# Performance work log

Measured on AMD Instinct MI355X. Metric: run time of the kernel, lower is better.

Reference implementation:

```python
import jax, jax.numpy as jnp
import numpy as np

E = 256      # embedding_dim
H = 8        # num_heads
D = E // H   # head_dim = 32
F = 1024     # dim_feedforward
EPS = 1e-5


def layer_norm(x, gamma, beta):
    mu = jnp.mean(x, axis=-1, keepdims=True)
    var = jnp.var(x, axis=-1, keepdims=True)
    return (x - mu) * jax.lax.rsqrt(var + EPS) * gamma + beta


def setup_inputs() -> dict:
    key = jax.random.key(0)
    ks = jax.random.split(key, 12)
    s = lambda fan_in: 1.0 / np.sqrt(fan_in)
    src = jax.random.normal(ks[0], (4, 2048, E), dtype=jnp.float32)
    w_in = jax.random.uniform(ks[1], (3 * E, E), minval=-s(E), maxval=s(E), dtype=jnp.float32)
    w_out = jax.random.uniform(ks[2], (E, E), minval=-s(E), maxval=s(E), dtype=jnp.float32)
    w1 = jax.random.uniform(ks[3], (F, E), minval=-s(E), maxval=s(E), dtype=jnp.float32)
    b1 = jax.random.uniform(ks[4], (F,), minval=-s(E), maxval=s(E), dtype=jnp.float32)
    w2 = jax.random.uniform(ks[5], (E, F), minval=-s(F), maxval=s(F), dtype=jnp.float32)
    b2 = jax.random.uniform(ks[6], (E,), minval=-s(F), maxval=s(F), dtype=jnp.float32)
    g1 = jnp.ones((E,), jnp.float32)
    beta1 = jnp.zeros((E,), jnp.float32)
    g2 = jnp.ones((E,), jnp.float32)
    beta2 = jnp.zeros((E,), jnp.float32)
    return {"src": src, "w_in": w_in, "w_out": w_out, "w1": w1, "b1": b1,
            "w2": w2, "b2": b2, "g1": g1, "beta1": beta1, "g2": g2, "beta2": beta2}


def reference(src, w_in, w_out, w1, b1, w2, b2, g1, beta1, g2, beta2):
    B, S, _ = src.shape
    scale = D ** (-0.5)
    # --- pre-norm self-attention block ---
    x = layer_norm(src, g1, beta1)                 # [B,S,E]
    qkv = x @ w_in.T                               # [B,S,3E]
    q, k, v = jnp.split(qkv, 3, axis=-1)
    q = q.reshape(B, S, H, D).transpose(0, 2, 1, 3)  # [B,H,S,D]
    k = k.reshape(B, S, H, D).transpose(0, 2, 1, 3)
    v = v.reshape(B, S, H, D).transpose(0, 2, 1, 3)
    scores = jnp.einsum('bhqd,bhkd->bhqk', q, k) * scale  # [B,H,S,S]
    attn = jax.nn.softmax(scores, axis=-1)
    out = jnp.einsum('bhqk,bhkd->bhqd', attn, v)   # [B,H,S,D]
    out = out.transpose(0, 2, 1, 3).reshape(B, S, E)
    src = src + out @ w_out.T
    # --- pre-norm FFN block ---
    y = layer_norm(src, g2, beta2)
    y = jax.nn.relu(y @ w1.T + b1) @ w2.T + b2
    return src + y
```

## Files before the change

### kernel.cpp

```cpp
#include <hip/hip_runtime.h>
#include <hip/hip_bf16.h>
#include <math.h>

typedef unsigned short u16;
typedef unsigned int   u32;
using bf16x8 = __attribute__((ext_vector_type(8))) short;
using f32x4  = __attribute__((ext_vector_type(4))) float;
using f32x16 = __attribute__((ext_vector_type(16))) float;
using u32v4  = __attribute__((ext_vector_type(4))) u32;

#define TE 256
#define TH 8
#define TS 2048
#define TB 4
#define NTOK 8192
#define QSCALE 0.2550120651552454f
#define EXP2(x) __builtin_amdgcn_exp2f(x)

__device__ __forceinline__ void async16(const u16* g, u16* l) {
    __builtin_amdgcn_global_load_lds(
        (const __attribute__((address_space(1))) u32*)g,
        (__attribute__((address_space(3))) u32*)l, 16, 0, 0);
}
__device__ __forceinline__ u32 pkbf(float a, float b) {
    u32 ua = __float_as_uint(a) + 0x8000u;
    u32 ub = __float_as_uint(b) + 0x8000u;
    return __builtin_amdgcn_perm(ub, ua, 0x07060302u);
}
__device__ __forceinline__ u16 bf1(float a) {
    return (u16)((__float_as_uint(a) + 0x8000u) >> 16);
}
template<int N> __device__ __forceinline__ void waitv() {
    if constexpr (N == 0)      asm volatile("s_waitcnt vmcnt(0)" ::: "memory");
    else if constexpr (N == 2) asm volatile("s_waitcnt vmcnt(2)" ::: "memory");
    else                       asm volatile("s_waitcnt vmcnt(4)" ::: "memory");
}

__global__ __launch_bounds__(256) void ln_bf(const float* __restrict__ in,
        u16* __restrict__ out, const float* __restrict__ gamma,
        const float* __restrict__ beta) {
    int row  = blockIdx.x * 4 + (threadIdx.x >> 6);
    int lane = threadIdx.x & 63;
    float4 v = ((const float4*)(in + (size_t)row * TE))[lane];
    float s  = v.x + v.y + v.z + v.w;
    float s2 = v.x*v.x + v.y*v.y + v.z*v.z + v.w*v.w;
    #pragma unroll
    for (int off = 32; off > 0; off >>= 1) {
        s  += __shfl_down(s,  off, 64);
        s2 += __shfl_down(s2, off, 64);
    }
    s  = __shfl(s,  0, 64);
    s2 = __shfl(s2, 0, 64);
    float mu = s * (1.f / TE);
    float rs = rsqrtf(s2 * (1.f / TE) - mu * mu + 1e-5f);
    float4 g = ((const float4*)gamma)[lane];
    float4 b = ((const float4*)beta )[lane];
    u32 lo = pkbf((v.x - mu) * rs * g.x + b.x, (v.y - mu) * rs * g.y + b.y);
    u32 hi = pkbf((v.z - mu) * rs * g.z + b.z, (v.w - mu) * rs * g.w + b.w);
    ((uint2*)(out + (size_t)row * TE))[lane] = make_uint2(lo, hi);
}

__global__ __launch_bounds__(256) void convw(const float* __restrict__ s0, u16* d0,
        const float* __restrict__ s1, u16* d1, const float* __restrict__ s2, u16* d2,
        const float* __restrict__ s3, u16* d3) {
    int i = (blockIdx.x * 256 + threadIdx.x) * 4;
    const float* s; u16* d;
    if      (i < 196608) { s = s0; d = d0; }
    else if (i < 262144) { s = s1; d = d1; i -= 196608; }
    else if (i < 524288) { s = s2; d = d2; i -= 262144; }
    else                 { s = s3; d = d3; i -= 524288; }
    float4 v = *(const float4*)(s + i);
    *(uint2*)(d + i) = make_uint2(pkbf(v.x, v.y), pkbf(v.z, v.w));
}

template<int K, int BM, int EPI>
__global__ __launch_bounds__(256) void mgemm(const u16* __restrict__ A,
        const u16* __restrict__ W, const float* __restrict__ bias,
        const float* __restrict__ R, float* __restrict__ Cf,
        u16* __restrict__ Cb, int M) {
    constexpr int BN = BM;
    constexpr int NS = K / 32;
    constexpr int L  = (BM == 128) ? 4 : 2;
    __shared__ u16 Al[3][BM * 32];
    __shared__ u16 Wl[3][BN * 32];
    const int tid = threadIdx.x, w = tid >> 6, l = tid & 63;
    const int n0 = blockIdx.y * BM;
    const int m0 = blockIdx.x * BN;
    constexpr int NT = (BM == 128) ? 4 : 2;
    constexpr int NF = (BM == 128) ? 4 : 2;
    const int tw = (w & 1) * NT * 16;
    const int fw = (w >> 1) * NF * 16;
    const int fr = l & 15, fq = l >> 4;
    const int sr = l >> 2, sc = (l & 3) * 8;
    f32x4 acc[NT][NF];
    #pragma unroll
    for (int t = 0; t < NT; t++)
        #pragma unroll
        for (int f = 0; f < NF; f++)
            #pragma unroll
            for (int r = 0; r < 4; r++) acc[t][f][r] = 0.f;

    auto stage = [&](int s, int buf) {
        const int kc = s * 32;
        if constexpr (BM == 128) {
            #pragma unroll
            for (int c = 0; c < 2; c++) {
                const int rr = (w * 2 + c) * 16 + sr;
                async16(A + (size_t)(n0 + rr) * K + kc + sc, &Al[buf][(w * 2 + c) * 512]);
                async16(W + (size_t)(m0 + rr) * K + kc + sc, &Wl[buf][(w * 2 + c) * 512]);
            }
        } else {
            const int rr = w * 16 + sr;
            async16(A + (size_t)(n0 + rr) * K + kc + sc, &Al[buf][w * 512]);
            async16(W + (size_t)(m0 + rr) * K + kc + sc, &Wl[buf][w * 512]);
        }
    };

    stage(0, 0);
    stage(1, 1);
    #pragma unroll
    for (int s = 0; s < NS; ++s) {
        const int buf = s % 3;
        if (s < NS - 1) waitv<L>();
        else            waitv<0>();
        __builtin_amdgcn_s_barrier();
        __builtin_amdgcn_sched_barrier(0);
        if (s + 2 < NS) stage(s + 2, (s + 2) % 3);
        bf16x8 af[NT], wf[NF];
        #pragma unroll
        for (int t = 0; t < NT; t++)
            af[t] = *(const bf16x8*)&Al[buf][(tw + t * 16 + fr) * 32 + fq * 8];
        #pragma unroll
        for (int f = 0; f < NF; f++)
            wf[f] = *(const bf16x8*)&Wl[buf][(fw + f * 16 + fr) * 32 + fq * 8];
        #pragma unroll
        for (int t = 0; t < NT; t++)
            #pragma unroll
            for (int f = 0; f < NF; f++)
                acc[t][f] = __builtin_amdgcn_mfma_f32_16x16x32_bf16(
                    wf[f], af[t], acc[t][f], 0, 0, 0);
    }
    #pragma unroll
    for (int t = 0; t < NT; t++) {
        const int tok = n0 + tw + t * 16 + fr;
        #pragma unroll
        for (int f = 0; f < NF; f++) {
            const int fb = m0 + fw + f * 16 + fq * 4;
            f32x4 v = acc[t][f];
            if (EPI == 0) {
                if (fb < 256) {
                    *(uint2*)(Cb + (size_t)tok * 256 + fb) = make_uint2(
                        pkbf(v[0]*QSCALE, v[1]*QSCALE), pkbf(v[2]*QSCALE, v[3]*QSCALE));
                } else if (fb < 512) {
                    const int hh = (fb - 256) >> 5, dd = (fb - 256) & 31;
                    const int bh = (tok >> 11) * 8 + hh;
                    const int kv = tok & 2047, tile = kv >> 5, lq = kv & 31;
                    const int fg = dd >> 4, hg = (dd >> 3) & 1, j = dd & 7;
                    u16* kp = (u16*)bias +
                        (((((size_t)bh * 64 + tile) * 2 + fg) * 2 + hg) * 32 + lq) * 8 + j;
                    *(uint2*)kp = make_uint2(pkbf(v[0], v[1]), pkbf(v[2], v[3]));
                } else {
                    const int hh = (fb - 512) >> 5, dd = (fb - 512) & 31;
                    const int bh = (tok >> 11) * 8 + hh;
                    const int kv = tok & 2047, tile = kv >> 5, kvr = kv & 31;
                    const int fg = kvr >> 4, hg = (kvr >> 3) & 1, j = kvr & 7;
                    u16* vp = (u16*)R +
                        ((((size_t)bh * 64 + tile) * 2 + fg) * 2 + hg) * 256 +
                        (size_t)dd * 8 + j;
                    vp[0]  = bf1(v[0]);
                    vp[8]  = bf1(v[1]);
                    vp[16] = bf1(v[2]);
                    vp[24] = bf1(v[3]);
                }
            } else if (EPI == 1) {
                float4 r4 = *(const float4*)(R + (size_t)tok * M + fb);
                *(float4*)(Cf + (size_t)tok * M + fb) =
                    make_float4(v[0]+r4.x, v[1]+r4.y, v[2]+r4.z, v[3]+r4.w);
            } else if (EPI == 2) {
                float4 b4 = *(const float4*)(bias + fb);
                *(uint2*)(Cb + (size_t)tok * M + fb) = make_uint2(
                    pkbf(fmaxf(v[0]+b4.x, 0.f), fmaxf(v[1]+b4.y, 0.f)),
                    pkbf(fmaxf(v[2]+b4.z, 0.f), fmaxf(v[3]+b4.w, 0.f)));
            } else {
                float4 b4 = *(const float4*)(bias + fb);
                float4 r4 = *(const float4*)(R + (size_t)tok * M + fb);
                *(float4*)(Cf + (size_t)tok * M + fb) = make_float4(
                    v[0]+b4.x+r4.x, v[1]+b4.y+r4.y, v[2]+b4.z+r4.z, v[3]+b4.w+r4.w);
            }
        }
    }
}

__global__ __launch_bounds__(256, 4) void attn_k(const u16* __restrict__ qb,
        const u16* __restrict__ kfb, const u16* __restrict__ vfb,
        u16* __restrict__ attn) {
    const int id = blockIdx.x;
    const int bh   = (id & 7) * 4 + (id >> 8);
    const int tile = (id >> 3) & 31;
    const int b = bh >> 3, h = bh & 7;
    const int tid = threadIdx.x, w = tid >> 6, l = tid & 63;
    const int qw = w & 1, kw = w >> 1;
    const int lq = l & 31, hi = l >> 5;
    const size_t btok = (size_t)b * TS;
    const int q0 = tile * 64 + qw * 32;

    __shared__ float mrg[2304];

    const u16* qrow = qb + (btok + q0 + lq) * 256 + h * 32 + hi * 8;
    bf16x8 qf0 = *(const bf16x8*)qrow;
    bf16x8 qf1 = *(const bf16x8*)(qrow + 16);

    f32x16 zf, o;
    #pragma unroll
    for (int r = 0; r < 16; r++) { zf[r] = 0.f; o[r] = 0.f; }
    float ps = 0.f;

    const u16* kp = kfb + ((size_t)bh * 64 + kw * 32) * 1024 + l * 8;
    const u16* vp = vfb + ((size_t)bh * 64 + kw * 32) * 1024 + l * 8;
    bf16x8 k0 = *(const bf16x8*)kp;
    bf16x8 k1 = *(const bf16x8*)(kp + 512);
    bf16x8 v0 = *(const bf16x8*)vp;
    bf16x8 v1 = *(const bf16x8*)(vp + 512);

    #pragma unroll 2
    for (int it = 0; it < 32; ++it) {
        kp += 1024; vp += 1024;
        bf16x8 nk0 = *(const bf16x8*)kp;
        bf16x8 nk1 = *(const bf16x8*)(kp + 512);
        bf16x8 nv0 = *(const bf16x8*)vp;
        bf16x8 nv1 = *(const bf16x8*)(vp + 512);
        f32x16 p = __builtin_amdgcn_mfma_f32_32x32x16_bf16(k0, qf0, zf, 0, 0, 0);
        p = __builtin_amdgcn_mfma_f32_32x32x16_bf16(k1, qf1, p, 0, 0, 0);
        float e[16];
        #pragma unroll
        for (int r = 0; r < 16; r++) e[r] = EXP2(p[r]);
        ps += ((e[0]+e[1]) + (e[2]+e[3])) + ((e[4]+e[5]) + (e[6]+e[7]))
            + ((e[8]+e[9]) + (e[10]+e[11])) + ((e[12]+e[13]) + (e[14]+e[15]));
        u32 a[8];
        #pragma unroll
        for (int j = 0; j < 8; j++)
            asm("v_cvt_pk_bf16_f32 %0, %1, %2"
                : "=v"(a[j]) : "v"(e[2*j]), "v"(e[2*j+1]));
        asm("v_permlane32_swap_b32 %0, %1" : "+v"(a[0]), "+v"(a[2]));
        asm("v_permlane32_swap_b32 %0, %1" : "+v"(a[1]), "+v"(a[3]));
        asm("v_permlane32_swap_b32 %0, %1" : "+v"(a[4]), "+v"(a[6]));
        asm("v_permlane32_swap_b32 %0, %1" : "+v"(a[5]), "+v"(a[7]));
        u32v4 t0 = {a[0], a[1], a[2], a[3]};
        u32v4 t1 = {a[4], a[5], a[6], a[7]};
        bf16x8 pf0 = __builtin_bit_cast(bf16x8, t0);
        bf16x8 pf1 = __builtin_bit_cast(bf16x8, t1);
        o = __builtin_amdgcn_mfma_f32_32x32x16_bf16(v0, pf0, o, 0, 0, 0);
        o = __builtin_amdgcn_mfma_f32_32x32x16_bf16(v1, pf1, o, 0, 0, 0);
        k0 = nk0; k1 = nk1; v0 = nv0; v1 = nv1;
    }
    ps += __shfl_xor(ps, 32, 64);

    if (kw == 1) {
        float* d = mrg + (qw * 64 + l) * 18;
        #pragma unroll
        for (int r = 0; r < 16; r++) d[r] = o[r];
        d[16] = ps;
    }
    __syncthreads();
    if (kw == 0) {
        const float* d = mrg + (qw * 64 + l) * 18;
        #pragma unroll
        for (int r = 0; r < 16; r++) o[r] += d[r];
        ps += d[16];
        float inv = 1.f / ps;
        int tok = (int)btok + q0 + lq;
        u16* orow = attn + (size_t)tok * 256 + h * 32 + hi * 4;
        #pragma unroll
        for (int g = 0; g < 4; g++)
            *(uint2*)(orow + g * 8) = make_uint2(
                pkbf(o[4*g]*inv, o[4*g+1]*inv), pkbf(o[4*g+2]*inv, o[4*g+3]*inv));
    }
}

extern "C" void kernel_launch(void* const* d_in, const int* in_sizes, int n_in,
                              void* d_out, int out_size, void* d_ws, size_t ws_size,
                              hipStream_t stream) {
    const float* src  = (const float*)d_in[0];
    const float* w_in = (const float*)d_in[1];
    const float* w_out= (const float*)d_in[2];
    const float* w1   = (const float*)d_in[3];
    const float* b1   = (const float*)d_in[4];
    const float* w2   = (const float*)d_in[5];
    const float* b2   = (const float*)d_in[6];
    const float* g1   = (const float*)d_in[7];
    const float* be1  = (const float*)d_in[8];
    const float* g2   = (const float*)d_in[9];
    const float* be2  = (const float*)d_in[10];
    float* out = (float*)d_out;

    u16* xb    = (u16*)d_ws;
    u16* qb    = xb + (size_t)NTOK * 256;
    u16* kfbuf = qb + (size_t)NTOK * 256;
    u16* vfbuf = kfbuf + (size_t)32 * 64 * 1024;
    u16* attnb = xb;
    u16* h1b   = (u16*)d_ws;
    u16* x2b   = (u16*)((char*)d_ws + (size_t)NTOK * 1024 * 2);
    u16* wib   = x2b + (size_t)NTOK * 256;
    u16* wob   = wib + 768 * 256;
    u16* w1b   = wob + 256 * 256;
    u16* w2b   = w1b + 1024 * 256;

    convw<<<768, 256, 0, stream>>>(w_in, wib, w_out, wob, w1, w1b, w2, w2b);
    ln_bf<<<NTOK / 4, 256, 0, stream>>>(src, xb, g1, be1);
    mgemm<256, 128, 0><<<dim3(6, 64), 256, 0, stream>>>(
        xb, wib, (const float*)kfbuf, (const float*)vfbuf, nullptr, qb, 768);
    attn_k<<<dim3(1024), 256, 0, stream>>>(qb, kfbuf, vfbuf, attnb);
    mgemm<256, 64, 1><<<dim3(4, 128), 256, 0, stream>>>(
        attnb, wob, nullptr, src, out, nullptr, 256);
    ln_bf<<<NTOK / 4, 256, 0, stream>>>(out, x2b, g2, be2);
    mgemm<256, 128, 2><<<dim3(8, 64), 256, 0, stream>>>(
        x2b, w1b, b1, nullptr, nullptr, h1b, 1024);
    mgemm<1024, 64, 3><<<dim3(4, 128), 256, 0, stream>>>(
        h1b, w2b, b2, out, out, nullptr, 256);
}
```

Before: 164.0 us.

## Fuse FFN GEMMs into one kernel keeping hidden activations in LDS

Replaces the two FFN GEMM launches with a single kernel. Each block computes relu(x·W1ᵀ+b1) for 32 tokens into shared memory, then multiplies by W2 and adds the bias and residual, so the 8192x1024 bf16 hidden tensor never goes through global memory. The weights are pre-permuted into MFMA fragment order in a merged prep kernel, which also absorbs the first LayerNorm launch. The trade-off is only 256 blocks of 32 tokens each, with weights streamed from global/L2 per block, so the work may be poorly parallelised and bandwidth-heavy on a large GPU.

```diff
diff --git a/kernel.cpp b/kernel.cpp
--- a/kernel.cpp
+++ b/kernel.cpp
@@ -36,10 +36,10 @@
     else                       asm volatile("s_waitcnt vmcnt(4)" ::: "memory");
 }
 
-__global__ __launch_bounds__(256) void ln_bf(const float* __restrict__ in,
+__device__ __forceinline__ void ln_body(const float* __restrict__ in,
         u16* __restrict__ out, const float* __restrict__ gamma,
-        const float* __restrict__ beta) {
-    int row  = blockIdx.x * 4 + (threadIdx.x >> 6);
+        const float* __restrict__ beta, int rowblk) {
+    int row  = rowblk * 4 + (threadIdx.x >> 6);
     int lane = threadIdx.x & 63;
     float4 v = ((const float4*)(in + (size_t)row * TE))[lane];
     float s  = v.x + v.y + v.z + v.w;
@@ -60,17 +60,45 @@
     ((uint2*)(out + (size_t)row * TE))[lane] = make_uint2(lo, hi);
 }
 
-__global__ __launch_bounds__(256) void convw(const float* __restrict__ s0, u16* d0,
-        const float* __restrict__ s1, u16* d1, const float* __restrict__ s2, u16* d2,
-        const float* __restrict__ s3, u16* d3) {
-    int i = (blockIdx.x * 256 + threadIdx.x) * 4;
-    const float* s; u16* d;
-    if      (i < 196608) { s = s0; d = d0; }
-    else if (i < 262144) { s = s1; d = d1; i -= 196608; }
-    else if (i < 524288) { s = s2; d = d2; i -= 262144; }
-    else                 { s = s3; d = d3; i -= 524288; }
-    float4 v = *(const float4*)(s + i);
-    *(uint2*)(d + i) = make_uint2(pkbf(v.x, v.y), pkbf(v.z, v.w));
+__global__ __launch_bounds__(256) void ln_bf(const float* __restrict__ in,
+        u16* __restrict__ out, const float* __restrict__ gamma,
+        const float* __restrict__ beta) {
+    ln_body(in, out, gamma, beta, blockIdx.x);
+}
+
+__global__ __launch_bounds__(256) void prep(const float* __restrict__ w_in, u16* wib,
+        const float* __restrict__ w_out, u16* wob, const float* __restrict__ w1,
+        u16* w1f, const float* __restrict__ w2, u16* w2f,
+        const float* __restrict__ src, u16* __restrict__ xb,
+        const float* __restrict__ g1, const float* __restrict__ be1) {
+    if (blockIdx.x < 768) {
+        int i = (blockIdx.x * 256 + threadIdx.x) * 4;
+        if (i < 196608) {
+            float4 v = *(const float4*)(w_in + i);
+            *(uint2*)(wib + i) = make_uint2(pkbf(v.x, v.y), pkbf(v.z, v.w));
+        } else if (i < 262144) {
+            int k = i - 196608;
+            float4 v = *(const float4*)(w_out + k);
+            *(uint2*)(wob + k) = make_uint2(pkbf(v.x, v.y), pkbf(v.z, v.w));
+        } else if (i < 524288) {
+            int k = i - 262144;
+            int f = k >> 8, c = k & 255;
+            int ft = f >> 5, fr = f & 31, kt = c >> 4, hi = (c >> 3) & 1, j = c & 7;
+            float4 v = *(const float4*)(w1 + k);
+            *(uint2*)(w1f + ft * 8192 + kt * 512 + hi * 256 + fr * 8 + j) =
+                make_uint2(pkbf(v.x, v.y), pkbf(v.z, v.w));
+        } else {
+            int k = i - 524288;
+            int e = k >> 10, c = k & 1023;
+            int ft = c >> 5, kt2 = (c >> 4) & 1, hi = (c >> 3) & 1, j = c & 7;
+            int et = e >> 5, er = e & 31;
+            float4 v = *(const float4*)(w2 + k);
+            *(uint2*)(w2f + ft * 8192 + kt2 * 4096 + et * 512 + hi * 256 + er * 8 + j) =
+                make_uint2(pkbf(v.x, v.y), pkbf(v.z, v.w));
+        }
+    } else {
+        ln_body(src, xb, g1, be1, blockIdx.x - 768);
+    }
 }
 
 template<int K, int BM, int EPI>
@@ -172,21 +200,111 @@
                     vp[16] = bf1(v[2]);
                     vp[24] = bf1(v[3]);
                 }
-            } else if (EPI == 1) {
+            } else {
                 float4 r4 = *(const float4*)(R + (size_t)tok * M + fb);
                 *(float4*)(Cf + (size_t)tok * M + fb) =
                     make_float4(v[0]+r4.x, v[1]+r4.y, v[2]+r4.z, v[3]+r4.w);
-            } else if (EPI == 2) {
-                float4 b4 = *(const float4*)(bias + fb);
-                *(uint2*)(Cb + (size_t)tok * M + fb) = make_uint2(
-                    pkbf(fmaxf(v[0]+b4.x, 0.f), fmaxf(v[1]+b4.y, 0.f)),
-                    pkbf(fmaxf(v[2]+b4.z, 0.f), fmaxf(v[3]+b4.w, 0.f)));
-            } else {
-                float4 b4 = *(const float4*)(bias + fb);
-                float4 r4 = *(const float4*)(R + (size_t)tok * M + fb);
-                *(float4*)(Cf + (size_t)tok * M + fb) = make_float4(
-                    v[0]+b4.x+r4.x, v[1]+b4.y+r4.y, v[2]+b4.z+r4.z, v[3]+b4.w+r4.w);
             }
+        }
+    }
+}
+
+__global__ __launch_bounds__(256) void ffn(const u16* __restrict__ x2b,
+        const u16* __restrict__ w1f, const float* __restrict__ b1,
+        const u16* __restrict__ w2f, const float* __restrict__ b2,
+        float* __restrict__ out) {
+    __shared__ u16 hl[32 * 2 * 512];
+    const int tid = threadIdx.x, w = tid >> 6, l = tid & 63;
+    const int lt = l & 31, hi = l >> 5;
+    const int tok0 = blockIdx.x * 32;
+
+    const u16* xrow = x2b + (size_t)(tok0 + lt) * 256 + hi * 8;
+    bf16x8 xf[16];
+    #pragma unroll
+    for (int kt = 0; kt < 16; kt++)
+        xf[kt] = *(const bf16x8*)(xrow + kt * 16);
+
+    #pragma unroll 2
+    for (int ftl = 0; ftl < 8; ++ftl) {
+        const int gft = w * 8 + ftl;
+        const u16* wp = w1f + gft * 8192 + l * 8;
+        bf16x8 wfr[16];
+        #pragma unroll
+        for (int kt = 0; kt < 16; kt++)
+            wfr[kt] = *(const bf16x8*)(wp + kt * 512);
+        f32x16 acc;
+        #pragma unroll
+        for (int r = 0; r < 16; r++) acc[r] = 0.f;
+        #pragma unroll
+        for (int kt = 0; kt < 16; kt++)
+            acc = __builtin_amdgcn_mfma_f32_32x32x16_bf16(wfr[kt], xf[kt], acc, 0, 0, 0);
+        const float* bb = b1 + gft * 32 + hi * 4;
+        float4 b0  = *(const float4*)(bb);
+        float4 b8  = *(const float4*)(bb + 8);
+        float4 b16 = *(const float4*)(bb + 16);
+        float4 b24 = *(const float4*)(bb + 24);
+        float t[16];
+        t[0]  = fmaxf(acc[0]  + b0.x,  0.f); t[1]  = fmaxf(acc[1]  + b0.y,  0.f);
+        t[2]  = fmaxf(acc[2]  + b0.z,  0.f); t[3]  = fmaxf(acc[3]  + b0.w,  0.f);
+        t[4]  = fmaxf(acc[4]  + b8.x,  0.f); t[5]  = fmaxf(acc[5]  + b8.y,  0.f);
+        t[6]  = fmaxf(acc[6]  + b8.z,  0.f); t[7]  = fmaxf(acc[7]  + b8.w,  0.f);
+        t[8]  = fmaxf(acc[8]  + b16.x, 0.f); t[9]  = fmaxf(acc[9]  + b16.y, 0.f);
+        t[10] = fmaxf(acc[10] + b16.z, 0.f); t[11] = fmaxf(acc[11] + b16.w, 0.f);
+        t[12] = fmaxf(acc[12] + b24.x, 0.f); t[13] = fmaxf(acc[13] + b24.y, 0.f);
+        t[14] = fmaxf(acc[14] + b24.z, 0.f); t[15] = fmaxf(acc[15] + b24.w, 0.f);
+        u32 a[8];
+        #pragma unroll
+        for (int j = 0; j < 8; j++)
+            asm("v_cvt_pk_bf16_f32 %0, %1, %2"
+                : "=v"(a[j]) : "v"(t[2*j]), "v"(t[2*j+1]));
+        asm("v_permlane32_swap_b32 %0, %1" : "+v"(a[0]), "+v"(a[2]));
+        asm("v_permlane32_swap_b32 %0, %1" : "+v"(a[1]), "+v"(a[3]));
+        asm("v_permlane32_swap_b32 %0, %1" : "+v"(a[4]), "+v"(a[6]));
+        asm("v_permlane32_swap_b32 %0, %1" : "+v"(a[5]), "+v"(a[7]));
+        u32v4 t0 = {a[0], a[1], a[2], a[3]};
+        u32v4 t1 = {a[4], a[5], a[6], a[7]};
+        u16* hp = &hl[(gft * 2) * 512 + l * 8];
+        *(u32v4*)hp = t0;
+        *(u32v4*)(hp + 512) = t1;
+    }
+    __syncthreads();
+    f32x16 o0, o1;
+    #pragma unroll
+    for (int r = 0; r < 16; r++) { o0[r] = 0.f; o1[r] = 0.f; }
+    #pragma unroll 2
+    for (int gft = 0; gft < 32; ++gft) {
+        #pragma unroll
+        for (int kt2 = 0; kt2 < 2; kt2++) {
+            bf16x8 hf = *(const bf16x8*)&hl[(gft * 2 + kt2) * 512 + l * 8];
+            const u16* w2p = w2f + gft * 8192 + kt2 * 4096 + (w * 2) * 512 + l * 8;
+            bf16x8 wa = *(const bf16x8*)w2p;
+            bf16x8 wb = *(const bf16x8*)(w2p + 512);
+            o0 = __builtin_amdgcn_mfma_f32_32x32x16_bf16(wa, hf, o0, 0, 0, 0);
+            o1 = __builtin_amdgcn_mfma_f32_32x32x16_bf16(wb, hf, o1, 0, 0, 0);
+        }
+    }
+    const int tok = tok0 + lt;
+    float* orow = out + (size_t)tok * 256;
+    {
+        const int e0 = (w * 2) * 32 + hi * 4;
+        #pragma unroll
+        for (int g = 0; g < 4; g++) {
+            float4 r4 = *(const float4*)(orow + e0 + g * 8);
+            float4 b4 = *(const float4*)(b2 + e0 + g * 8);
+            *(float4*)(orow + e0 + g * 8) = make_float4(
+                o0[4*g] + r4.x + b4.x, o0[4*g+1] + r4.y + b4.y,
+                o0[4*g+2] + r4.z + b4.z, o0[4*g+3] + r4.w + b4.w);
+        }
+    }
+    {
+        const int e0 = (w * 2 + 1) * 32 + hi * 4;
+        #pragma unroll
+        for (int g = 0; g < 4; g++) {
+            float4 r4 = *(const float4*)(orow + e0 + g * 8);
+            float4 b4 = *(const float4*)(b2 + e0 + g * 8);
+            *(float4*)(orow + e0 + g * 8) = make_float4(
+                o1[4*g] + r4.x + b4.x, o1[4*g+1] + r4.y + b4.y,
+                o1[4*g+2] + r4.z + b4.z, o1[4*g+3] + r4.w + b4.w);
         }
     }
 }
@@ -298,23 +416,19 @@
     u16* kfbuf = qb + (size_t)NTOK * 256;
     u16* vfbuf = kfbuf + (size_t)32 * 64 * 1024;
     u16* attnb = xb;
-    u16* h1b   = (u16*)d_ws;
     u16* x2b   = (u16*)((char*)d_ws + (size_t)NTOK * 1024 * 2);
     u16* wib   = x2b + (size_t)NTOK * 256;
     u16* wob   = wib + 768 * 256;
-    u16* w1b   = wob + 256 * 256;
-    u16* w2b   = w1b + 1024 * 256;
-
-    convw<<<768, 256, 0, stream>>>(w_in, wib, w_out, wob, w1, w1b, w2, w2b);
-    ln_bf<<<NTOK / 4, 256, 0, stream>>>(src, xb, g1, be1);
+    u16* w1fb  = wob + 256 * 256;
+    u16* w2fb  = w1fb + 1024 * 256;
+
+    prep<<<768 + NTOK / 4, 256, 0, stream>>>(
+        w_in, wib, w_out, wob, w1, w1fb, w2, w2fb, src, xb, g1, be1);
     mgemm<256, 128, 0><<<dim3(6, 64), 256, 0, stream>>>(
         xb, wib, (const float*)kfbuf, (const float*)vfbuf, nullptr, qb, 768);
     attn_k<<<dim3(1024), 256, 0, stream>>>(qb, kfbuf, vfbuf, attnb);
     mgemm<256, 64, 1><<<dim3(4, 128), 256, 0, stream>>>(
         attnb, wob, nullptr, src, out, nullptr, 256);
     ln_bf<<<NTOK / 4, 256, 0, stream>>>(out, x2b, g2, be2);
-    mgemm<256, 128, 2><<<dim3(8, 64), 256, 0, stream>>>(
-        x2b, w1b, b1, nullptr, nullptr, h1b, 1024);
-    mgemm<1024, 64, 3><<<dim3(4, 128), 256, 0, stream>>>(
-        h1b, w2b, b2, out, out, nullptr, 256);
-}
+    ffn<<<256, 256, 0, stream>>>(x2b, w1fb, b1, w2fb, b2, out);
+}
```

After: 171.5 us. 1.05x slower.
